# Kernel tuning notes

Measured on AMD Instinct MI355X. Metric: run time of the kernel, lower is better.

Reference implementation:

```python
import jax, jax.numpy as jnp
import numpy as np

N = 50000      # nodes
E = 400000     # edges (before self loops)
F_IN = 128     # num_features
HID = 64       # hidden_dim
HEADS = 4
G = 64         # number of graphs in batch
NCLS = 2
NEG = 0.2      # leaky relu negative slope
BN_EPS = 1e-5


def setup_inputs() -> dict:
    key = jax.random.key(0)
    ks = jax.random.split(key, 32)
    rn = lambda k, shape, s=0.05: jax.random.normal(k, shape, jnp.float32) * s
    inp = {}
    inp["x"] = jax.random.normal(ks[0], (N, F_IN), jnp.float32)
    inp["edge_index"] = jax.random.randint(ks[1], (2, E), 0, N, dtype=jnp.int32)
    inp["batch"] = jnp.sort(jax.random.randint(ks[2], (N,), 0, G, dtype=jnp.int32))
    # layer 0 GATConv (concat=True) + pre projection
    inp["conv0_W"] = rn(ks[3], (F_IN, HEADS * HID))
    inp["conv0_att_src"] = rn(ks[4], (HEADS, HID))
    inp["conv0_att_dst"] = rn(ks[5], (HEADS, HID))
    inp["conv0_bias"] = jnp.zeros((HEADS * HID,), jnp.float32)
    inp["pre0_W"] = rn(ks[6], (HEADS * HID, HID))
    inp["pre0_b"] = jnp.zeros((HID,), jnp.float32)
    # layers 1..2 GATConv (concat=False), stacked
    inp["convs_W"] = rn(ks[7], (2, HID, HEADS * HID))
    inp["convs_att_src"] = rn(ks[8], (2, HEADS, HID))
    inp["convs_att_dst"] = rn(ks[9], (2, HEADS, HID))
    inp["convs_bias"] = jnp.zeros((2, HID), jnp.float32)
    # batch norms (eval mode: running stats)
    inp["bn_gamma"] = jnp.ones((3, HID), jnp.float32)
    inp["bn_beta"] = jnp.zeros((3, HID), jnp.float32)
    inp["bn_mean"] = rn(ks[10], (3, HID), 0.1)
    inp["bn_var"] = jax.random.uniform(ks[11], (3, HID), jnp.float32) + 0.5
    # JK projection, attention pooling, classifier
    inp["jump_W"] = rn(ks[12], (3 * HID, HID))
    inp["jump_b"] = jnp.zeros((HID,), jnp.float32)
    inp["att_W"] = rn(ks[13], (HID, 1))
    inp["att_b"] = jnp.zeros((1,), jnp.float32)
    inp["cls_W1"] = rn(ks[14], (HID, HID // 2))
    inp["cls_b1"] = jnp.zeros((HID // 2,), jnp.float32)
    inp["cls_W2"] = rn(ks[15], (HID // 2, NCLS))
    inp["cls_b2"] = jnp.zeros((NCLS,), jnp.float32)
    return inp


def _segment_softmax(logits, seg, num_segments):
    m = jax.ops.segment_max(logits, seg, num_segments=num_segments)
    e = jnp.exp(logits - m[seg])
    s = jax.ops.segment_sum(e, seg, num_segments=num_segments)
    return e / s[seg]


def _gat_conv(x, src, dst, W, a_src, a_dst, bias, concat):
    n = x.shape[0]
    H, C = a_src.shape
    xh = (x @ W).reshape(n, H, C)                         # [N, H, C]
    as_n = jnp.einsum('nhc,hc->nh', xh, a_src)            # [N, H]
    ad_n = jnp.einsum('nhc,hc->nh', xh, a_dst)            # [N, H]
    logits = jax.nn.leaky_relu(as_n[src] + ad_n[dst], NEG)  # [E', H]
    att = _segment_softmax(logits, dst, n)                # softmax over incoming edges
    out = jax.ops.segment_sum(xh[src] * att[:, :, None], dst, num_segments=n)
    out = out.reshape(n, H * C) if concat else out.mean(axis=1)
    return out + bias


def _bn(h, g, b, m, v):
    return (h - m) * jax.lax.rsqrt(v + BN_EPS) * g + b


def reference(x, edge_index, batch, conv0_W, conv0_att_src, conv0_att_dst,
              conv0_bias, pre0_W, pre0_b, convs_W, convs_att_src, convs_att_dst,
              convs_bias, bn_gamma, bn_beta, bn_mean, bn_var, jump_W, jump_b,
              att_W, att_b, cls_W1, cls_b1, cls_W2, cls_b2):
    n = x.shape[0]
    loops = jnp.arange(n, dtype=edge_index.dtype)
    src = jnp.concatenate([edge_index[0], loops])         # add_self_loops=True
    dst = jnp.concatenate([edge_index[1], loops])
    reps = []
    # layer 0: concat heads -> pre projection -> BN -> ELU (no residual: 128 != 64)
    h = _gat_conv(x, src, dst, conv0_W, conv0_att_src, conv0_att_dst, conv0_bias, True)
    h = h @ pre0_W + pre0_b
    h = jax.nn.elu(_bn(h, bn_gamma[0], bn_beta[0], bn_mean[0], bn_var[0]))
    reps.append(h)
    # layers 1..2: mean heads -> BN -> ELU -> residual
    for i in range(2):
        h_in = h
        h = _gat_conv(h, src, dst, convs_W[i], convs_att_src[i], convs_att_dst[i],
                      convs_bias[i], False)
        h = jax.nn.elu(_bn(h, bn_gamma[i + 1], bn_beta[i + 1], bn_mean[i + 1], bn_var[i + 1]))
        h = h + h_in
        reps.append(h)
    # jumping knowledge (cat)
    h = jnp.concatenate(reps, axis=-1) @ jump_W + jump_b  # [N, HID]
    # attentional global pooling
    a = _segment_softmax((h @ att_W + att_b)[:, 0], batch, G)  # [N]
    hg = jax.ops.segment_sum(h * a[:, None], batch, num_segments=G)  # [G, HID]
    # classifier
    return jax.nn.relu(hg @ cls_W1 + cls_b1) @ cls_W2 + cls_b2
```

## Files before the change

kernel.cpp:

```cpp
#include <hip/hip_runtime.h>
#include <hip/hip_bf16.h>
#include <math.h>

#define NEG 0.2f
#define BNEPS 1e-5f
#define NGRAPH 64
#define SCAN_CHUNK 2048
#define POOL_BLOCKS 256

typedef short bf16x8 __attribute__((ext_vector_type(8)));
typedef float f32x4  __attribute__((ext_vector_type(4)));
typedef float f32x2  __attribute__((ext_vector_type(2)));

__device__ __forceinline__ float bf2f(unsigned short u) {
    return __uint_as_float(((unsigned)u) << 16);
}
__device__ __forceinline__ short f2bf(float f) {
    return (short)__bfloat16_as_ushort(__float2bfloat16(f));
}
__device__ __forceinline__ unsigned char f2fp8(float f) {
    int pk = __builtin_amdgcn_cvt_pk_fp8_f32(f, f, 0, false);
    return (unsigned char)(pk & 0xFF);
}

__global__ __launch_bounds__(256)
void init_kernel(const int* __restrict__ batch, int N,
                 int* __restrict__ counts, int* __restrict__ gstart,
                 float* __restrict__ hg_acc, float* __restrict__ wsum_acc,
                 const float* __restrict__ convs_W,
                 const float* __restrict__ convs_as, const float* __restrict__ convs_ad,
                 float* __restrict__ uv)
{
    int idx = blockIdx.x * 256 + threadIdx.x;
    for (int i = idx; i < N; i += gridDim.x * 256) counts[i] = 0;
    if (blockIdx.x == 0) {
        int t = threadIdx.x;
        for (int i = t; i < NGRAPH * 64; i += 256) hg_acc[i] = 0.f;
        if (t < NGRAPH) wsum_acc[t] = 0.f;
        if (t <= NGRAPH) {
            int lo = 0, hi = N;
            while (lo < hi) {
                int mid = (lo + hi) >> 1;
                if (batch[mid] < t) lo = mid + 1; else hi = mid;
            }
            gstart[t] = lo;
        }
    }
    if (blockIdx.x == 1) {
        int t = threadIdx.x;
        int h = t >> 6, k = t & 63;
        for (int i = 0; i < 2; ++i) {
            const float* Wr  = convs_W + (size_t)i * 64 * 256 + k * 256 + h * 64;
            const float* av  = convs_as + i * 256 + h * 64;
            const float* dv  = convs_ad + i * 256 + h * 64;
            float su = 0.f, sv = 0.f;
            for (int c = 0; c < 64; ++c) { su += Wr[c] * av[c]; sv += Wr[c] * dv[c]; }
            uv[i * 256 + h * 64 + k]       = su;
            uv[512 + i * 256 + h * 64 + k] = sv;
        }
    }
}

__global__ __launch_bounds__(256)
void gemm_xh_mfma(const float* __restrict__ A, int lda,
                  const float* __restrict__ W, int Nc, int M, int K,
                  const float* __restrict__ att_s, const float* __restrict__ att_d,
                  float* __restrict__ as_out, float* __restrict__ ad_out,
                  unsigned char* __restrict__ C8)
{
    __shared__ short Wt[64 * 136];
    const int KP = K + 8;
    int tid  = threadIdx.x;
    int lane = tid & 63, wave = tid >> 6;
    int row0 = blockIdx.x * 64;
    int colb = blockIdx.y * 64;
    int c15 = lane & 15, q = lane >> 4;

    {
        int n = tid & 63;
        for (int k = tid >> 6; k < K; k += 4)
            Wt[n * KP + k] = f2bf(W[(size_t)k * Nc + colb + n]);
    }
    __syncthreads();

    int row = row0 + wave * 16 + c15;
    bool rok = row < M;
    const float* arow = A + (size_t)row * lda + q * 8;

    f32x4 acc[4];
    #pragma unroll
    for (int st = 0; st < 4; ++st) acc[st] = (f32x4){0.f, 0.f, 0.f, 0.f};

    for (int k0 = 0; k0 < K; k0 += 32) {
        bf16x8 av;
        if (rok) {
            float4 a0 = *(const float4*)(arow + k0);
            float4 a1 = *(const float4*)(arow + k0 + 4);
            av[0] = f2bf(a0.x); av[1] = f2bf(a0.y); av[2] = f2bf(a0.z); av[3] = f2bf(a0.w);
            av[4] = f2bf(a1.x); av[5] = f2bf(a1.y); av[6] = f2bf(a1.z); av[7] = f2bf(a1.w);
        } else {
            av = (bf16x8){0,0,0,0,0,0,0,0};
        }
        #pragma unroll
        for (int st = 0; st < 4; ++st) {
            bf16x8 bv = *(const bf16x8*)(Wt + (st * 16 + c15) * KP + k0 + q * 8);
            acc[st] = __builtin_amdgcn_mfma_f32_16x16x32_bf16(av, bv, acc[st], 0, 0, 0);
        }
    }

    #pragma unroll
    for (int r = 0; r < 4; ++r) {
        int orow = row0 + wave * 16 + q * 4 + r;
        if (orow >= M) continue;
        unsigned char* cb = C8 + (size_t)orow * 256 + colb + c15;
        #pragma unroll
        for (int st = 0; st < 4; ++st)
            cb[st * 16] = f2fp8(acc[st][r]);
    }
    float sa[4], da[4];
    #pragma unroll
    for (int st = 0; st < 4; ++st) {
        sa[st] = att_s[colb + st * 16 + c15];
        da[st] = att_d[colb + st * 16 + c15];
    }
    #pragma unroll
    for (int r = 0; r < 4; ++r) {
        float ps = acc[0][r] * sa[0] + acc[1][r] * sa[1] + acc[2][r] * sa[2] + acc[3][r] * sa[3];
        float pd = acc[0][r] * da[0] + acc[1][r] * da[1] + acc[2][r] * da[2] + acc[3][r] * da[3];
        #pragma unroll
        for (int o = 1; o < 16; o <<= 1) {
            ps += __shfl_xor(ps, o);
            pd += __shfl_xor(pd, o);
        }
        int orow = row0 + wave * 16 + q * 4 + r;
        if (c15 == 0 && orow < M) {
            as_out[orow * 4 + blockIdx.y] = ps;
            ad_out[orow * 4 + blockIdx.y] = pd;
        }
    }
}

__global__ __launch_bounds__(256)
void gemm_n64_mfma(const void* __restrict__ Araw, int lda, int a_is_bf16,
                   const float* __restrict__ W, int w_gat, int M, int K,
                   const float* __restrict__ bias, float scale,
                   float* __restrict__ C, int ldc, int mode,
                   const float* __restrict__ bn_g, const float* __restrict__ bn_b,
                   const float* __restrict__ bn_m, const float* __restrict__ bn_v,
                   const float* __restrict__ resid, int ldr,
                   unsigned char* __restrict__ h8_out,
                   const float* __restrict__ u, const float* __restrict__ v,
                   float* __restrict__ as_out, float* __restrict__ ad_out,
                   const float* __restrict__ attW, const float* __restrict__ attb,
                   float* __restrict__ wout)
{
    __shared__ short Wt[64 * 264];
    const int KP = K + 8;
    int tid  = threadIdx.x;
    int lane = tid & 63, wave = tid >> 6;
    int row0 = blockIdx.x * 64;
    int c15 = lane & 15, q = lane >> 4;

    {
        int n = tid & 63;
        for (int k = tid >> 6; k < K; k += 4) {
            int widx = w_gat ? ((k & 63) * 256 + (k >> 6) * 64 + n) : (k * 64 + n);
            Wt[n * KP + k] = f2bf(W[widx]);
        }
    }
    __syncthreads();

    int row = row0 + wave * 16 + c15;
    bool rok = row < M;

    f32x4 acc[4];
    #pragma unroll
    for (int st = 0; st < 4; ++st) acc[st] = (f32x4){0.f, 0.f, 0.f, 0.f};

    for (int k0 = 0; k0 < K; k0 += 32) {
        bf16x8 av;
        if (rok) {
            if (a_is_bf16) {
                av = *(const bf16x8*)((const unsigned short*)Araw
                                      + (size_t)row * lda + k0 + q * 8);
            } else {
                const float* ap = (const float*)Araw + (size_t)row * lda + k0 + q * 8;
                float4 a0 = *(const float4*)ap;
                float4 a1 = *(const float4*)(ap + 4);
                av[0] = f2bf(a0.x); av[1] = f2bf(a0.y); av[2] = f2bf(a0.z); av[3] = f2bf(a0.w);
                av[4] = f2bf(a1.x); av[5] = f2bf(a1.y); av[6] = f2bf(a1.z); av[7] = f2bf(a1.w);
            }
        } else {
            av = (bf16x8){0,0,0,0,0,0,0,0};
        }
        #pragma unroll
        for (int st = 0; st < 4; ++st) {
            bf16x8 bv = *(const bf16x8*)(Wt + (st * 16 + c15) * KP + k0 + q * 8);
            acc[st] = __builtin_amdgcn_mfma_f32_16x16x32_bf16(av, bv, acc[st], 0, 0, 0);
        }
    }

    #pragma unroll
    for (int st = 0; st < 4; ++st) {
        int col = st * 16 + c15;
        float bs = bias ? bias[col] : 0.f;
        float sg = 1.f, sb = 0.f;
        if (mode == 1) {
            sg = bn_g[col] / sqrtf(bn_v[col] + BNEPS);
            sb = bn_b[col] - bn_m[col] * sg;
        }
        #pragma unroll
        for (int r = 0; r < 4; ++r) {
            int orow = row0 + wave * 16 + q * 4 + r;
            if (orow >= M) continue;
            float vvv = acc[st][r] * scale + bs;
            if (mode == 1) {
                vvv = vvv * sg + sb;
                vvv = vvv > 0.f ? vvv : __expf(vvv) - 1.f;
            }
            if (resid) vvv += resid[(size_t)orow * ldr + col];
            acc[st][r] = vvv;
            C[(size_t)orow * ldc + col] = vvv;
        }
    }

    if (h8_out) {
        #pragma unroll
        for (int r = 0; r < 4; ++r) {
            int orow = row0 + wave * 16 + q * 4 + r;
            if (orow >= M) continue;
            unsigned char* hb = h8_out + (size_t)orow * 64 + c15;
            #pragma unroll
            for (int st = 0; st < 4; ++st)
                hb[st * 16] = f2fp8(acc[st][r]);
        }
    }

    if (u) {
        float uu[4][4], vv2[4][4];
        #pragma unroll
        for (int h = 0; h < 4; ++h)
            #pragma unroll
            for (int st = 0; st < 4; ++st) {
                uu[h][st]  = u[h * 64 + st * 16 + c15];
                vv2[h][st] = v[h * 64 + st * 16 + c15];
            }
        #pragma unroll
        for (int r = 0; r < 4; ++r) {
            int orow = row0 + wave * 16 + q * 4 + r;
            float pv[8];
            #pragma unroll
            for (int h = 0; h < 4; ++h) {
                pv[h]     = acc[0][r] * uu[h][0] + acc[1][r] * uu[h][1]
                          + acc[2][r] * uu[h][2] + acc[3][r] * uu[h][3];
                pv[4 + h] = acc[0][r] * vv2[h][0] + acc[1][r] * vv2[h][1]
                          + acc[2][r] * vv2[h][2] + acc[3][r] * vv2[h][3];
            }
            #pragma unroll
            for (int j = 0; j < 4; ++j) {
                float send = (c15 & 8) ? pv[j] : pv[j + 4];
                float keep = (c15 & 8) ? pv[j + 4] : pv[j];
                pv[j] = keep + __shfl_xor(send, 8);
            }
            #pragma unroll
            for (int j = 0; j < 2; ++j) {
                float send = (c15 & 4) ? pv[j] : pv[j + 2];
                float keep = (c15 & 4) ? pv[j + 2] : pv[j];
                pv[j] = keep + __shfl_xor(send, 4);
            }
            {
                float send = (c15 & 2) ? pv[0] : pv[1];
                float keep = (c15 & 2) ? pv[1] : pv[0];
                pv[0] = keep + __shfl_xor(send, 2);
            }
            pv[0] += __shfl_xor(pv[0], 1);
            if ((c15 & 1) == 0 && orow < M) {
                int jj = c15 >> 1;
                if (jj < 4) as_out[orow * 4 + jj] = pv[0];
                else        ad_out[orow * 4 + (jj - 4)] = pv[0];
            }
        }
    }

    if (wout) {
        float sa[4];
        #pragma unroll
        for (int st = 0; st < 4; ++st) sa[st] = attW[st * 16 + c15];
        float ab = attb[0];
        #pragma unroll
        for (int r = 0; r < 4; ++r) {
            float ps = acc[0][r] * sa[0] + acc[1][r] * sa[1]
                     + acc[2][r] * sa[2] + acc[3][r] * sa[3];
            #pragma unroll
            for (int o = 1; o < 16; o <<= 1) ps += __shfl_xor(ps, o);
            int orow = row0 + wave * 16 + q * 4 + r;
            if (c15 == 0 && orow < M) wout[orow] = __expf(ps + ab);
        }
    }
}

__global__ __launch_bounds__(256)
void hist_kernel(const int* __restrict__ ei, int E, int N, int* __restrict__ counts)
{
    int e = blockIdx.x * blockDim.x + threadIdx.x;
    int Etot = E + N;
    if (e >= Etot) return;
    int d = (e < E) ? ei[E + e] : e - E;
    atomicAdd(&counts[d], 1);
}

__global__ __launch_bounds__(256)
void scan_phase1(const int* __restrict__ counts, int N, int* __restrict__ blocksum)
{
    __shared__ int wsum[4];
    int tid = threadIdx.x, lane = tid & 63, wave = tid >> 6;
    int base = blockIdx.x * SCAN_CHUNK;
    int s = 0;
    #pragma unroll
    for (int j = 0; j < SCAN_CHUNK / 256; ++j) {
        int idx = base + tid + j * 256;
        if (idx < N) s += counts[idx];
    }
    #pragma unroll
    for (int o = 32; o; o >>= 1) s += __shfl_xor(s, o);
    if (lane == 0) wsum[wave] = s;
    __syncthreads();
    if (tid == 0) blocksum[blockIdx.x] = wsum[0] + wsum[1] + wsum[2] + wsum[3];
}

__global__ __launch_bounds__(256)
void scan_phase3(const int* __restrict__ counts, int N, int nb,
                 const int* __restrict__ blocksum,
                 int* __restrict__ rowptr, int* __restrict__ cursor)
{
    __shared__ int wsum[4];
    __shared__ int pref[64];
    int tid = threadIdx.x, lane = tid & 63, wave = tid >> 6;

    if (wave == 0) {
        int v = (lane < nb) ? blocksum[lane] : 0;
        int incl = v;
        #pragma unroll
        for (int o = 1; o < 64; o <<= 1) {
            int t = __shfl_up(incl, o);
            if (lane >= o) incl += t;
        }
        pref[lane] = incl;
    }
    __syncthreads();
    int boff = blockIdx.x ? pref[blockIdx.x - 1] : 0;
    if (blockIdx.x == 0 && tid == 0) rowptr[N] = pref[nb - 1];

    int start = blockIdx.x * SCAN_CHUNK + tid * 8;
    int v[8];
    int s = 0;
    #pragma unroll
    for (int j = 0; j < 8; ++j) {
        v[j] = (start + j < N) ? counts[start + j] : 0;
        s += v[j];
    }
    int incl = s;
    #pragma unroll
    for (int o = 1; o < 64; o <<= 1) {
        int t = __shfl_up(incl, o);
        if (lane >= o) incl += t;
    }
    if (lane == 63) wsum[wave] = incl;
    __syncthreads();
    int woff = 0;
    #pragma unroll
    for (int w = 0; w < 4; ++w) if (w < wave) woff += wsum[w];
    int run = boff + woff + incl - s;
    #pragma unroll
    for (int j = 0; j < 8; ++j) {
        int idx = start + j;
        if (idx < N) { rowptr[idx] = run; cursor[idx] = run; }
        run += v[j];
    }
}

__global__ __launch_bounds__(256)
void scatter_kernel(const int* __restrict__ ei, int E, int N,
                    int* __restrict__ cursor, int* __restrict__ csr_src)
{
    int e = blockIdx.x * blockDim.x + threadIdx.x;
    int Etot = E + N;
    if (e >= Etot) return;
    int s, d;
    if (e < E) { s = ei[e]; d = ei[E + e]; } else { s = d = e - E; }
    int pos = atomicAdd(&cursor[d], 1);
    csr_src[pos] = s;
}

__global__ __launch_bounds__(256)
void aggregate_kernel(const int* __restrict__ rowptr, const int* __restrict__ csr_src,
                      const float* __restrict__ as_n, const float* __restrict__ ad_n,
                      const unsigned char* __restrict__ xh8,
                      const float* __restrict__ bias,
                      unsigned short* __restrict__ outp, int N)
{
    int node = (blockIdx.x * blockDim.x + threadIdx.x) >> 6;
    int lane = threadIdx.x & 63;
    if (node >= N) return;
    int h = lane >> 4, li = lane & 15, grp = lane & 48;
    int e0 = rowptr[node], e1 = rowptr[node + 1];
    float adh = ad_n[node * 4 + h];
    unsigned laneoff = (unsigned)(lane * 4);

    float4 acc = make_float4(0.f, 0.f, 0.f, 0.f);
    float wsum = 0.f;

    for (int base = e0; base < e1; base += 16) {
        int cnt = e1 - base; if (cnt > 16) cnt = 16;
        int s = 0; float w = 0.f;
        if (li < cnt) {
            s = csr_src[base + li];
            float l = as_n[s * 4 + h] + adh;
            l = fmaxf(l, NEG * l);
            w = __expf(l);
        }
        int k = 0;
        for (; k + 3 < cnt; k += 4) {
            float w0 = __shfl(w, grp + k),     w1 = __shfl(w, grp + k + 1);
            float w2 = __shfl(w, grp + k + 2), w3 = __shfl(w, grp + k + 3);
            int s0 = __shfl(s, grp + k),       s1 = __shfl(s, grp + k + 1);
            int s2 = __shfl(s, grp + k + 2),   s3 = __shfl(s, grp + k + 3);
            unsigned x0 = *(const unsigned*)(xh8 + ((unsigned)s0 * 256u + laneoff));
            unsigned x1 = *(const unsigned*)(xh8 + ((unsigned)s1 * 256u + laneoff));
            unsigned x2 = *(const unsigned*)(xh8 + ((unsigned)s2 * 256u + laneoff));
            unsigned x3 = *(const unsigned*)(xh8 + ((unsigned)s3 * 256u + laneoff));
            f32x2 l0 = __builtin_amdgcn_cvt_pk_f32_fp8((int)x0, false);
            f32x2 h0 = __builtin_amdgcn_cvt_pk_f32_fp8((int)x0, true);
            f32x2 l1 = __builtin_amdgcn_cvt_pk_f32_fp8((int)x1, false);
            f32x2 h1 = __builtin_amdgcn_cvt_pk_f32_fp8((int)x1, true);
            f32x2 l2 = __builtin_amdgcn_cvt_pk_f32_fp8((int)x2, false);
            f32x2 h2 = __builtin_amdgcn_cvt_pk_f32_fp8((int)x2, true);
            f32x2 l3 = __builtin_amdgcn_cvt_pk_f32_fp8((int)x3, false);
            f32x2 h3 = __builtin_amdgcn_cvt_pk_f32_fp8((int)x3, true);
            acc.x += w0 * l0.x; acc.y += w0 * l0.y; acc.z += w0 * h0.x; acc.w += w0 * h0.y;
            acc.x += w1 * l1.x; acc.y += w1 * l1.y; acc.z += w1 * h1.x; acc.w += w1 * h1.y;
            acc.x += w2 * l2.x; acc.y += w2 * l2.y; acc.z += w2 * h2.x; acc.w += w2 * h2.y;
            acc.x += w3 * l3.x; acc.y += w3 * l3.y; acc.z += w3 * h3.x; acc.w += w3 * h3.y;
            wsum += (w0 + w1) + (w2 + w3);
        }
        for (; k < cnt; ++k) {
            float wk = __shfl(w, grp + k);
            int sk = __shfl(s, grp + k);
            unsigned xv = *(const unsigned*)(xh8 + ((unsigned)sk * 256u + laneoff));
            f32x2 lo = __builtin_amdgcn_cvt_pk_f32_fp8((int)xv, false);
            f32x2 hi = __builtin_amdgcn_cvt_pk_f32_fp8((int)xv, true);
            acc.x += wk * lo.x; acc.y += wk * lo.y;
            acc.z += wk * hi.x; acc.w += wk * hi.y;
            wsum += wk;
        }
    }

    float rw = 1.f / wsum;
    float4 bs = *(const float4*)(bias + lane * 4);
    ushort4 pk;
    pk.x = (unsigned short)f2bf(acc.x * rw + bs.x);
    pk.y = (unsigned short)f2bf(acc.y * rw + bs.y);
    pk.z = (unsigned short)f2bf(acc.z * rw + bs.z);
    pk.w = (unsigned short)f2bf(acc.w * rw + bs.w);
    *(ushort4*)(outp + (size_t)node * 256 + lane * 4) = pk;
}

__global__ __launch_bounds__(256)
void aggregate_z(const int* __restrict__ rowptr, const int* __restrict__ csr_src,
                 const float* __restrict__ as_n, const float* __restrict__ ad_n,
                 const unsigned char* __restrict__ h8,
                 unsigned short* __restrict__ zout, int N)
{
    int node = (blockIdx.x * blockDim.x + threadIdx.x) >> 6;
    int lane = threadIdx.x & 63;
    if (node >= N) return;
    int h = lane >> 4, li = lane & 15, grp = lane & 48;
    int e0 = rowptr[node], e1 = rowptr[node + 1];
    float adh = ad_n[node * 4 + h];
    unsigned laneoff = (unsigned)(li * 4);

    float4 acc = make_float4(0.f, 0.f, 0.f, 0.f);
    float wsum = 0.f;

    for (int base = e0; base < e1; base += 16) {
        int cnt = e1 - base; if (cnt > 16) cnt = 16;
        int s = 0; float w = 0.f;
        if (li < cnt) {
            s = csr_src[base + li];
            float l = as_n[s * 4 + h] + adh;
            l = fmaxf(l, NEG * l);
            w = __expf(l);
        }
        int k = 0;
        for (; k + 3 < cnt; k += 4) {
            float w0 = __shfl(w, grp + k),     w1 = __shfl(w, grp + k + 1);
            float w2 = __shfl(w, grp + k + 2), w3 = __shfl(w, grp + k + 3);
            int s0 = __shfl(s, grp + k),       s1 = __shfl(s, grp + k + 1);
            int s2 = __shfl(s, grp + k + 2),   s3 = __shfl(s, grp + k + 3);
            unsigned x0 = *(const unsigned*)(h8 + ((unsigned)s0 * 64u + laneoff));
            unsigned x1 = *(const unsigned*)(h8 + ((unsigned)s1 * 64u + laneoff));
            unsigned x2 = *(const unsigned*)(h8 + ((unsigned)s2 * 64u + laneoff));
            unsigned x3 = *(const unsigned*)(h8 + ((unsigned)s3 * 64u + laneoff));
            f32x2 l0 = __builtin_amdgcn_cvt_pk_f32_fp8((int)x0, false);
            f32x2 h0 = __builtin_amdgcn_cvt_pk_f32_fp8((int)x0, true);
            f32x2 l1 = __builtin_amdgcn_cvt_pk_f32_fp8((int)x1, false);
            f32x2 h1 = __builtin_amdgcn_cvt_pk_f32_fp8((int)x1, true);
            f32x2 l2 = __builtin_amdgcn_cvt_pk_f32_fp8((int)x2, false);
            f32x2 h2 = __builtin_amdgcn_cvt_pk_f32_fp8((int)x2, true);
            f32x2 l3 = __builtin_amdgcn_cvt_pk_f32_fp8((int)x3, false);
            f32x2 h3 = __builtin_amdgcn_cvt_pk_f32_fp8((int)x3, true);
            acc.x += w0 * l0.x; acc.y += w0 * l0.y; acc.z += w0 * h0.x; acc.w += w0 * h0.y;
            acc.x += w1 * l1.x; acc.y += w1 * l1.y; acc.z += w1 * h1.x; acc.w += w1 * h1.y;
            acc.x += w2 * l2.x; acc.y += w2 * l2.y; acc.z += w2 * h2.x; acc.w += w2 * h2.y;
            acc.x += w3 * l3.x; acc.y += w3 * l3.y; acc.z += w3 * h3.x; acc.w += w3 * h3.y;
            wsum += (w0 + w1) + (w2 + w3);
        }
        for (; k < cnt; ++k) {
            float wk = __shfl(w, grp + k);
            int sk = __shfl(s, grp + k);
            unsigned xv = *(const unsigned*)(h8 + ((unsigned)sk * 64u + laneoff));
            f32x2 lo = __builtin_amdgcn_cvt_pk_f32_fp8((int)xv, false);
            f32x2 hi = __builtin_amdgcn_cvt_pk_f32_fp8((int)xv, true);
            acc.x += wk * lo.x; acc.y += wk * lo.y;
            acc.z += wk * hi.x; acc.w += wk * hi.y;
            wsum += wk;
        }
    }

    float rw = 1.f / wsum;
    ushort4 pk;
    pk.x = (unsigned short)f2bf(acc.x * rw);
    pk.y = (unsigned short)f2bf(acc.y * rw);
    pk.z = (unsigned short)f2bf(acc.z * rw);
    pk.w = (unsigned short)f2bf(acc.w * rw);
    *(ushort4*)(zout + (size_t)node * 256 + h * 64 + li * 4) = pk;
}

__global__ __launch_bounds__(256)
void pool_partial(const float* __restrict__ hjk, const float* __restrict__ w,
                  const int* __restrict__ batch, const int* __restrict__ gstart,
                  float* __restrict__ hg_acc, float* __restrict__ wsum_acc, int N)
{
    __shared__ float red[256];
    __shared__ float wred[4];
    int tid = threadIdx.x;
    int c = tid & 63, q = tid >> 6;
    int slab = (N + POOL_BLOCKS - 1) / POOL_BLOCKS;
    int n0 = blockIdx.x * slab;
    int n1 = n0 + slab; if (n1 > N) n1 = N;
    if (n0 >= n1) return;
    int g0 = batch[n0], g1 = batch[n1 - 1];

    for (int g = g0; g <= g1; ++g) {
        int s = gstart[g];     if (s < n0) s = n0;
        int e = gstart[g + 1]; if (e > n1) e = n1;
        float acc = 0.f, ws = 0.f;
        for (int n = s + q; n < e; n += 4) {
            float wn = w[n];
            acc += wn * hjk[(size_t)n * 64 + c];
            if (c == 0) ws += wn;
        }
        red[tid] = acc;
        if (c == 0) wred[q] = ws;
        __syncthreads();
        if (q == 0) {
            float v = red[c] + red[64 + c] + red[128 + c] + red[192 + c];
            if (v != 0.f) atomicAdd(&hg_acc[g * 64 + c], v);
            if (c == 0) {
                float t = wred[0] + wred[1] + wred[2] + wred[3];
                if (t != 0.f) atomicAdd(&wsum_acc[g], t);
            }
        }
        __syncthreads();
    }
}

__global__ void cls_kernel(const float* __restrict__ hg_acc,
                           const float* __restrict__ wsum_acc,
                           const float* __restrict__ W1, const float* __restrict__ b1,
                           const float* __restrict__ W2, const float* __restrict__ b2,
                           float* __restrict__ out)
{
    int g = blockIdx.x, t = threadIdx.x;
    __shared__ float z[32];
    __shared__ float h[64];
    float wsum = wsum_acc[g];
    float rw = (wsum > 0.f) ? 1.f / wsum : 0.f;
    h[t] = hg_acc[g * 64 + t] * rw;
    h[t + 32] = hg_acc[g * 64 + t + 32] * rw;
    __syncthreads();
    float acc = b1[t];
    for (int k = 0; k < 64; ++k) acc += h[k] * W1[k * 32 + t];
    z[t] = fmaxf(acc, 0.f);
    __syncthreads();
    if (t < 2) {
        float o = b2[t];
        for (int j = 0; j < 32; ++j) o += z[j] * W2[j * 2 + t];
        out[g * 2 + t] = o;
    }
}

extern "C" void kernel_launch(void* const* d_in, const int* in_sizes, int n_in,
                              void* d_out, int out_size, void* d_ws, size_t ws_size,
                              hipStream_t stream)
{
    const float* x        = (const float*)d_in[0];
    const int*   ei       = (const int*)d_in[1];
    const int*   batch    = (const int*)d_in[2];
    const float* conv0_W  = (const float*)d_in[3];
    const float* conv0_as = (const float*)d_in[4];
    const float* conv0_ad = (const float*)d_in[5];
    const float* conv0_b  = (const float*)d_in[6];
    const float* pre0_W   = (const float*)d_in[7];
    const float* pre0_b   = (const float*)d_in[8];
    const float* convs_W  = (const float*)d_in[9];
    const float* convs_as = (const float*)d_in[10];
    const float* convs_ad = (const float*)d_in[11];
    const float* convs_b  = (const float*)d_in[12];
    const float* bn_g     = (const float*)d_in[13];
    const float* bn_b     = (const float*)d_in[14];
    const float* bn_m     = (const float*)d_in[15];
    const float* bn_v     = (const float*)d_in[16];
    const float* jump_W   = (const float*)d_in[17];
    const float* jump_b   = (const float*)d_in[18];
    const float* att_W    = (const float*)d_in[19];
    const float* att_b    = (const float*)d_in[20];
    const float* cls_W1   = (const float*)d_in[21];
    const float* cls_b1   = (const float*)d_in[22];
    const float* cls_W2   = (const float*)d_in[23];
    const float* cls_b2   = (const float*)d_in[24];
    float* out = (float*)d_out;

    const int N = in_sizes[0] / 128;
    const int E = in_sizes[1] / 2;
    const int Etot = E + N;
    const int nb = (N + SCAN_CHUNK - 1) / SCAN_CHUNK;

    float* ws      = (float*)d_ws;
    unsigned char* xh8      = (unsigned char*)ws;
    unsigned short* h256_bf = (unsigned short*)ws + (size_t)N * 256;
    float* repsAll = (float*)(h256_bf + (size_t)N * 256);
    float* as_n    = repsAll + (size_t)N * 192;
    float* ad_n    = as_n + (size_t)N * 4;
    float* hjk     = ad_n + (size_t)N * 4;
    float* hg_acc  = hjk + (size_t)N * 64;
    float* wsum_acc= hg_acc + NGRAPH * 64;
    int*   rowptr  = (int*)(wsum_acc + NGRAPH);
    int*   cursor  = rowptr + (N + 1);
    int*   counts  = cursor + N;
    int*   csr_src = counts + N;
    int*   gstart  = csr_src + Etot;
    int*   blocksum = gstart + (NGRAPH + 1);
    float* uv      = (float*)(blocksum + 64);
    unsigned char* h8 = xh8;
    float* wbuf    = as_n;

    dim3 blk(256);
    int node_wave_blocks = (N + 3) / 4;
    int edge_blocks      = (Etot + 255) / 256;
    int row_blocks       = (N + 63) / 64;

    init_kernel<<<64, blk, 0, stream>>>(batch, N, counts, gstart, hg_acc, wsum_acc,
                                        convs_W, convs_as, convs_ad, uv);
    hist_kernel<<<edge_blocks, blk, 0, stream>>>(ei, E, N, counts);
    scan_phase1<<<nb, blk, 0, stream>>>(counts, N, blocksum);
    scan_phase3<<<nb, blk, 0, stream>>>(counts, N, nb, blocksum, rowptr, cursor);
    scatter_kernel<<<edge_blocks, blk, 0, stream>>>(ei, E, N, cursor, csr_src);

    {
        dim3 g1(row_blocks, 4);
        gemm_xh_mfma<<<g1, blk, 0, stream>>>(x, 128, conv0_W, 256, N, 128,
                                             conv0_as, conv0_ad, as_n, ad_n, xh8);
        aggregate_kernel<<<node_wave_blocks, blk, 0, stream>>>(
            rowptr, csr_src, as_n, ad_n, xh8, conv0_b, h256_bf, N);
        gemm_n64_mfma<<<row_blocks, blk, 0, stream>>>(
            h256_bf, 256, 1, pre0_W, 0, N, 256, pre0_b, 1.f,
            repsAll, 192, 1, bn_g, bn_b, bn_m, bn_v,
            nullptr, 0, h8, uv, uv + 512, as_n, ad_n,
            nullptr, nullptr, nullptr);
    }

    aggregate_z<<<node_wave_blocks, blk, 0, stream>>>(rowptr, csr_src, as_n, ad_n,
                                                      h8, h256_bf, N);
    gemm_n64_mfma<<<row_blocks, blk, 0, stream>>>(
        h256_bf, 256, 1, convs_W, 1, N, 256, convs_b, 0.25f,
        repsAll + 64, 192, 1, bn_g + 64, bn_b + 64, bn_m + 64, bn_v + 64,
        repsAll, 192, h8, uv + 256, uv + 512 + 256, as_n, ad_n,
        nullptr, nullptr, nullptr);

    aggregate_z<<<node_wave_blocks, blk, 0, stream>>>(rowptr, csr_src, as_n, ad_n,
                                                      h8, h256_bf, N);
    gemm_n64_mfma<<<row_blocks, blk, 0, stream>>>(
        h256_bf, 256, 1, convs_W + (size_t)64 * 256, 1, N, 256, convs_b + 64, 0.25f,
        repsAll + 128, 192, 1, bn_g + 128, bn_b + 128, bn_m + 128, bn_v + 128,
        repsAll + 64, 192, nullptr, nullptr, nullptr, nullptr, nullptr,
        nullptr, nullptr, nullptr);

    gemm_n64_mfma<<<row_blocks, blk, 0, stream>>>(
        repsAll, 192, 0, jump_W, 0, N, 192, jump_b, 1.f,
        hjk, 64, 0, nullptr, nullptr, nullptr, nullptr,
        nullptr, 0, nullptr, nullptr, nullptr, nullptr, nullptr,
        att_W, att_b, wbuf);

    pool_partial<<<POOL_BLOCKS, blk, 0, stream>>>(hjk, wbuf, batch, gstart,
                                                  hg_acc, wsum_acc, N);
    cls_kernel<<<NGRAPH, 32, 0, stream>>>(hg_acc, wsum_acc, cls_W1, cls_b1,
                                          cls_W2, cls_b2, out);
}
```

Measured before the change: 366.2 us.

## Fuse z-space aggregation with mean-head GEMM epilogue for layers one and two

Replaces the separate aggregate_z and gemm_n64 launches for the two mean-head GAT layers with one kernel. Each block aggregates 64 nodes into a shared-memory bf16 tile, then runs the MFMA GEMM with the BN/ELU/residual and attention-projection epilogue. This removes the N×256 bf16 intermediate round trip through global memory and two launches. The cost is serial per-wave aggregation of 16 nodes with less parallelism per block, large LDS use that lowers occupancy, and ping-pong h8/as/ad buffers to avoid read-write races between blocks.

New measurement: 452.7 us. 1.24x slower.

```diff
diff --git a/kernel.cpp b/kernel.cpp
--- a/kernel.cpp
+++ b/kernel.cpp
@@ -295,6 +295,195 @@
             for (int o = 1; o < 16; o <<= 1) ps += __shfl_xor(ps, o);
             int orow = row0 + wave * 16 + q * 4 + r;
             if (c15 == 0 && orow < M) wout[orow] = __expf(ps + ab);
+        }
+    }
+}
+
+__global__ __launch_bounds__(256)
+void agg_gemm_z(const int* __restrict__ rowptr, const int* __restrict__ csr_src,
+                const float* __restrict__ as_n, const float* __restrict__ ad_n,
+                const unsigned char* __restrict__ hsrc,
+                const float* __restrict__ W,
+                int M,
+                const float* __restrict__ bias, float scale,
+                float* __restrict__ C, int ldc,
+                const float* __restrict__ bn_g, const float* __restrict__ bn_b,
+                const float* __restrict__ bn_m, const float* __restrict__ bn_v,
+                const float* __restrict__ resid, int ldr,
+                unsigned char* __restrict__ h8_out,
+                const float* __restrict__ u, const float* __restrict__ v,
+                float* __restrict__ as_out, float* __restrict__ ad_out)
+{
+    __shared__ short zbuf[64 * 264];
+    __shared__ short Wt[64 * 136];
+    int tid  = threadIdx.x;
+    int lane = tid & 63, wave = tid >> 6;
+    int row0 = blockIdx.x * 64;
+    int h = lane >> 4, li = lane & 15, grp = lane & 48;
+    int c15 = lane & 15, q = lane >> 4;
+    unsigned laneoff = (unsigned)(li * 4);
+
+    for (int i = 0; i < 16; ++i) {
+        int node = row0 + wave * 16 + i;
+        int nl = wave * 16 + i;
+        float4 acc = make_float4(0.f, 0.f, 0.f, 0.f);
+        float wsum = 0.f;
+        if (node < M) {
+            float adh = ad_n[node * 4 + h];
+            int e0 = rowptr[node], e1 = rowptr[node + 1];
+            for (int base = e0; base < e1; base += 16) {
+                int cnt = e1 - base; if (cnt > 16) cnt = 16;
+                int s = 0; float w = 0.f;
+                if (li < cnt) {
+                    s = csr_src[base + li];
+                    float l = as_n[s * 4 + h] + adh;
+                    l = fmaxf(l, NEG * l);
+                    w = __expf(l);
+                }
+                int k = 0;
+                for (; k + 3 < cnt; k += 4) {
+                    float w0 = __shfl(w, grp + k),     w1 = __shfl(w, grp + k + 1);
+                    float w2 = __shfl(w, grp + k + 2), w3 = __shfl(w, grp + k + 3);
+                    int s0 = __shfl(s, grp + k),       s1 = __shfl(s, grp + k + 1);
+                    int s2 = __shfl(s, grp + k + 2),   s3 = __shfl(s, grp + k + 3);
+                    unsigned x0 = *(const unsigned*)(hsrc + ((unsigned)s0 * 64u + laneoff));
+                    unsigned x1 = *(const unsigned*)(hsrc + ((unsigned)s1 * 64u + laneoff));
+                    unsigned x2 = *(const unsigned*)(hsrc + ((unsigned)s2 * 64u + laneoff));
+                    unsigned x3 = *(const unsigned*)(hsrc + ((unsigned)s3 * 64u + laneoff));
+                    f32x2 l0 = __builtin_amdgcn_cvt_pk_f32_fp8((int)x0, false);
+                    f32x2 h0 = __builtin_amdgcn_cvt_pk_f32_fp8((int)x0, true);
+                    f32x2 l1 = __builtin_amdgcn_cvt_pk_f32_fp8((int)x1, false);
+                    f32x2 h1 = __builtin_amdgcn_cvt_pk_f32_fp8((int)x1, true);
+                    f32x2 l2 = __builtin_amdgcn_cvt_pk_f32_fp8((int)x2, false);
+                    f32x2 h2 = __builtin_amdgcn_cvt_pk_f32_fp8((int)x2, true);
+                    f32x2 l3 = __builtin_amdgcn_cvt_pk_f32_fp8((int)x3, false);
+                    f32x2 h3 = __builtin_amdgcn_cvt_pk_f32_fp8((int)x3, true);
+                    acc.x += w0 * l0.x; acc.y += w0 * l0.y; acc.z += w0 * h0.x; acc.w += w0 * h0.y;
+                    acc.x += w1 * l1.x; acc.y += w1 * l1.y; acc.z += w1 * h1.x; acc.w += w1 * h1.y;
+                    acc.x += w2 * l2.x; acc.y += w2 * l2.y; acc.z += w2 * h2.x; acc.w += w2 * h2.y;
+                    acc.x += w3 * l3.x; acc.y += w3 * l3.y; acc.z += w3 * h3.x; acc.w += w3 * h3.y;
+                    wsum += (w0 + w1) + (w2 + w3);
+                }
+                for (; k < cnt; ++k) {
+                    float wk = __shfl(w, grp + k);
+                    int sk = __shfl(s, grp + k);
+                    unsigned xv = *(const unsigned*)(hsrc + ((unsigned)sk * 64u + laneoff));
+                    f32x2 lo = __builtin_amdgcn_cvt_pk_f32_fp8((int)xv, false);
+                    f32x2 hi = __builtin_amdgcn_cvt_pk_f32_fp8((int)xv, true);
+                    acc.x += wk * lo.x; acc.y += wk * lo.y;
+                    acc.z += wk * hi.x; acc.w += wk * hi.y;
+                    wsum += wk;
+                }
+            }
+        }
+        float rw = (wsum > 0.f) ? 1.f / wsum : 0.f;
+        ushort4 pk;
+        pk.x = (unsigned short)f2bf(acc.x * rw);
+        pk.y = (unsigned short)f2bf(acc.y * rw);
+        pk.z = (unsigned short)f2bf(acc.z * rw);
+        pk.w = (unsigned short)f2bf(acc.w * rw);
+        *(ushort4*)((unsigned short*)zbuf + nl * 264 + lane * 4) = pk;
+    }
+
+    f32x4 acc2[4];
+    #pragma unroll
+    for (int st = 0; st < 4; ++st) acc2[st] = (f32x4){0.f, 0.f, 0.f, 0.f};
+
+    for (int kh = 0; kh < 2; ++kh) {
+        __syncthreads();
+        {
+            int n = tid & 63;
+            for (int k = tid >> 6; k < 128; k += 4) {
+                int kk = kh * 128 + k;
+                Wt[n * 136 + k] = f2bf(W[(kk & 63) * 256 + (kk >> 6) * 64 + n]);
+            }
+        }
+        __syncthreads();
+        const unsigned short* zb = (const unsigned short*)zbuf;
+        for (int k0 = 0; k0 < 128; k0 += 32) {
+            bf16x8 av = *(const bf16x8*)(zb + (wave * 16 + c15) * 264 + kh * 128 + k0 + q * 8);
+            #pragma unroll
+            for (int st = 0; st < 4; ++st) {
+                bf16x8 bv = *(const bf16x8*)(Wt + (st * 16 + c15) * 136 + k0 + q * 8);
+                acc2[st] = __builtin_amdgcn_mfma_f32_16x16x32_bf16(av, bv, acc2[st], 0, 0, 0);
+            }
+        }
+    }
+
+    #pragma unroll
+    for (int st = 0; st < 4; ++st) {
+        int col = st * 16 + c15;
+        float bs = bias[col];
+        float sg = bn_g[col] / sqrtf(bn_v[col] + BNEPS);
+        float sb = bn_b[col] - bn_m[col] * sg;
+        #pragma unroll
+        for (int r = 0; r < 4; ++r) {
+            int orow = row0 + wave * 16 + q * 4 + r;
+            if (orow >= M) continue;
+            float vvv = acc2[st][r] * scale + bs;
+            vvv = vvv * sg + sb;
+            vvv = vvv > 0.f ? vvv : __expf(vvv) - 1.f;
+            vvv += resid[(size_t)orow * ldr + col];
+            acc2[st][r] = vvv;
+            C[(size_t)orow * ldc + col] = vvv;
+        }
+    }
+
+    if (h8_out) {
+        #pragma unroll
+        for (int r = 0; r < 4; ++r) {
+            int orow = row0 + wave * 16 + q * 4 + r;
+            if (orow >= M) continue;
+            unsigned char* hb = h8_out + (size_t)orow * 64 + c15;
+            #pragma unroll
+            for (int st = 0; st < 4; ++st)
+                hb[st * 16] = f2fp8(acc2[st][r]);
+        }
+    }
+
+    if (u) {
+        float uu[4][4], vv2[4][4];
+        #pragma unroll
+        for (int hh = 0; hh < 4; ++hh)
+            #pragma unroll
+            for (int st = 0; st < 4; ++st) {
+                uu[hh][st]  = u[hh * 64 + st * 16 + c15];
+                vv2[hh][st] = v[hh * 64 + st * 16 + c15];
+            }
+        #pragma unroll
+        for (int r = 0; r < 4; ++r) {
+            int orow = row0 + wave * 16 + q * 4 + r;
+            float pv[8];
+            #pragma unroll
+            for (int hh = 0; hh < 4; ++hh) {
+                pv[hh]     = acc2[0][r] * uu[hh][0] + acc2[1][r] * uu[hh][1]
+                           + acc2[2][r] * uu[hh][2] + acc2[3][r] * uu[hh][3];
+                pv[4 + hh] = acc2[0][r] * vv2[hh][0] + acc2[1][r] * vv2[hh][1]
+                           + acc2[2][r] * vv2[hh][2] + acc2[3][r] * vv2[hh][3];
+            }
+            #pragma unroll
+            for (int j = 0; j < 4; ++j) {
+                float send = (c15 & 8) ? pv[j] : pv[j + 4];
+                float keep = (c15 & 8) ? pv[j + 4] : pv[j];
+                pv[j] = keep + __shfl_xor(send, 8);
+            }
+            #pragma unroll
+            for (int j = 0; j < 2; ++j) {
+                float send = (c15 & 4) ? pv[j] : pv[j + 2];
+                float keep = (c15 & 4) ? pv[j + 2] : pv[j];
+                pv[j] = keep + __shfl_xor(send, 4);
+            }
+            {
+                float send = (c15 & 2) ? pv[0] : pv[1];
+                float keep = (c15 & 2) ? pv[1] : pv[0];
+                pv[0] = keep + __shfl_xor(send, 2);
+            }
+            pv[0] += __shfl_xor(pv[0], 1);
+            if ((c15 & 1) == 0 && orow < M) {
+                int jj = c15 >> 1;
+                if (jj < 4) as_out[orow * 4 + jj] = pv[0];
+                else        ad_out[orow * 4 + (jj - 4)] = pv[0];
+            }
         }
     }
 }
@@ -463,77 +652,6 @@
     pk.z = (unsigned short)f2bf(acc.z * rw + bs.z);
     pk.w = (unsigned short)f2bf(acc.w * rw + bs.w);
     *(ushort4*)(outp + (size_t)node * 256 + lane * 4) = pk;
-}
-
-__global__ __launch_bounds__(256)
-void aggregate_z(const int* __restrict__ rowptr, const int* __restrict__ csr_src,
-                 const float* __restrict__ as_n, const float* __restrict__ ad_n,
-                 const unsigned char* __restrict__ h8,
-                 unsigned short* __restrict__ zout, int N)
-{
-    int node = (blockIdx.x * blockDim.x + threadIdx.x) >> 6;
-    int lane = threadIdx.x & 63;
-    if (node >= N) return;
-    int h = lane >> 4, li = lane & 15, grp = lane & 48;
-    int e0 = rowptr[node], e1 = rowptr[node + 1];
-    float adh = ad_n[node * 4 + h];
-    unsigned laneoff = (unsigned)(li * 4);
-
-    float4 acc = make_float4(0.f, 0.f, 0.f, 0.f);
-    float wsum = 0.f;
-
-    for (int base = e0; base < e1; base += 16) {
-        int cnt = e1 - base; if (cnt > 16) cnt = 16;
-        int s = 0; float w = 0.f;
-        if (li < cnt) {
-            s = csr_src[base + li];
-            float l = as_n[s * 4 + h] + adh;
-            l = fmaxf(l, NEG * l);
-            w = __expf(l);
-        }
-        int k = 0;
-        for (; k + 3 < cnt; k += 4) {
-            float w0 = __shfl(w, grp + k),     w1 = __shfl(w, grp + k + 1);
-            float w2 = __shfl(w, grp + k + 2), w3 = __shfl(w, grp + k + 3);
-            int s0 = __shfl(s, grp + k),       s1 = __shfl(s, grp + k + 1);
-            int s2 = __shfl(s, grp + k + 2),   s3 = __shfl(s, grp + k + 3);
-            unsigned x0 = *(const unsigned*)(h8 + ((unsigned)s0 * 64u + laneoff));
-            unsigned x1 = *(const unsigned*)(h8 + ((unsigned)s1 * 64u + laneoff));
-            unsigned x2 = *(const unsigned*)(h8 + ((unsigned)s2 * 64u + laneoff));
-            unsigned x3 = *(const unsigned*)(h8 + ((unsigned)s3 * 64u + laneoff));
-            f32x2 l0 = __builtin_amdgcn_cvt_pk_f32_fp8((int)x0, false);
-            f32x2 h0 = __builtin_amdgcn_cvt_pk_f32_fp8((int)x0, true);
-            f32x2 l1 = __builtin_amdgcn_cvt_pk_f32_fp8((int)x1, false);
-            f32x2 h1 = __builtin_amdgcn_cvt_pk_f32_fp8((int)x1, true);
-            f32x2 l2 = __builtin_amdgcn_cvt_pk_f32_fp8((int)x2, false);
-            f32x2 h2 = __builtin_amdgcn_cvt_pk_f32_fp8((int)x2, true);
-            f32x2 l3 = __builtin_amdgcn_cvt_pk_f32_fp8((int)x3, false);
-            f32x2 h3 = __builtin_amdgcn_cvt_pk_f32_fp8((int)x3, true);
-            acc.x += w0 * l0.x; acc.y += w0 * l0.y; acc.z += w0 * h0.x; acc.w += w0 * h0.y;
-            acc.x += w1 * l1.x; acc.y += w1 * l1.y; acc.z += w1 * h1.x; acc.w += w1 * h1.y;
-            acc.x += w2 * l2.x; acc.y += w2 * l2.y; acc.z += w2 * h2.x; acc.w += w2 * h2.y;
-            acc.x += w3 * l3.x; acc.y += w3 * l3.y; acc.z += w3 * h3.x; acc.w += w3 * h3.y;
-            wsum += (w0 + w1) + (w2 + w3);
-        }
-        for (; k < cnt; ++k) {
-            float wk = __shfl(w, grp + k);
-            int sk = __shfl(s, grp + k);
-            unsigned xv = *(const unsigned*)(h8 + ((unsigned)sk * 64u + laneoff));
-            f32x2 lo = __builtin_amdgcn_cvt_pk_f32_fp8((int)xv, false);
-            f32x2 hi = __builtin_amdgcn_cvt_pk_f32_fp8((int)xv, true);
-            acc.x += wk * lo.x; acc.y += wk * lo.y;
-            acc.z += wk * hi.x; acc.w += wk * hi.y;
-            wsum += wk;
-        }
-    }
-
-    float rw = 1.f / wsum;
-    ushort4 pk;
-    pk.x = (unsigned short)f2bf(acc.x * rw);
-    pk.y = (unsigned short)f2bf(acc.y * rw);
-    pk.z = (unsigned short)f2bf(acc.z * rw);
-    pk.w = (unsigned short)f2bf(acc.w * rw);
-    *(ushort4*)(zout + (size_t)node * 256 + h * 64 + li * 4) = pk;
 }
 
 __global__ __launch_bounds__(256)
@@ -652,7 +770,10 @@
     int*   gstart  = csr_src + Etot;
     int*   blocksum = gstart + (NGRAPH + 1);
     float* uv      = (float*)(blocksum + 64);
-    unsigned char* h8 = xh8;
+    float* as2     = uv + 1024;
+    float* ad2     = as2 + (size_t)N * 4;
+    unsigned char* h8b = (unsigned char*)(ad2 + (size_t)N * 4);
+    unsigned char* h8a = xh8;
     float* wbuf    = as_n;
 
     dim3 blk(256);
@@ -676,25 +797,25 @@
         gemm_n64_mfma<<<row_blocks, blk, 0, stream>>>(
             h256_bf, 256, 1, pre0_W, 0, N, 256, pre0_b, 1.f,
             repsAll, 192, 1, bn_g, bn_b, bn_m, bn_v,
-            nullptr, 0, h8, uv, uv + 512, as_n, ad_n,
+            nullptr, 0, h8a, uv, uv + 512, as_n, ad_n,
             nullptr, nullptr, nullptr);
     }
 
-    aggregate_z<<<node_wave_blocks, blk, 0, stream>>>(rowptr, csr_src, as_n, ad_n,
-                                                      h8, h256_bf, N);
-    gemm_n64_mfma<<<row_blocks, blk, 0, stream>>>(
-        h256_bf, 256, 1, convs_W, 1, N, 256, convs_b, 0.25f,
-        repsAll + 64, 192, 1, bn_g + 64, bn_b + 64, bn_m + 64, bn_v + 64,
-        repsAll, 192, h8, uv + 256, uv + 512 + 256, as_n, ad_n,
-        nullptr, nullptr, nullptr);
-
-    aggregate_z<<<node_wave_blocks, blk, 0, stream>>>(rowptr, csr_src, as_n, ad_n,
-                                                      h8, h256_bf, N);
-    gemm_n64_mfma<<<row_blocks, blk, 0, stream>>>(
-        h256_bf, 256, 1, convs_W + (size_t)64 * 256, 1, N, 256, convs_b + 64, 0.25f,
-        repsAll + 128, 192, 1, bn_g + 128, bn_b + 128, bn_m + 128, bn_v + 128,
-        repsAll + 64, 192, nullptr, nullptr, nullptr, nullptr, nullptr,
-        nullptr, nullptr, nullptr);
+    agg_gemm_z<<<row_blocks, blk, 0, stream>>>(
+        rowptr, csr_src, as_n, ad_n, h8a,
+        convs_W, N, convs_b, 0.25f,
+        repsAll + 64, 192,
+        bn_g + 64, bn_b + 64, bn_m + 64, bn_v + 64,
+        repsAll, 192,
+        h8b, uv + 256, uv + 512 + 256, as2, ad2);
+
+    agg_gemm_z<<<row_blocks, blk, 0, stream>>>(
+        rowptr, csr_src, as2, ad2, h8b,
+        convs_W + (size_t)64 * 256, N, convs_b + 64, 0.25f,
+        repsAll + 128, 192,
+        bn_g + 128, bn_b + 128, bn_m + 128, bn_v + 128,
+        repsAll + 64, 192,
+        nullptr, nullptr, nullptr, nullptr, nullptr);
 
     gemm_n64_mfma<<<row_blocks, blk, 0, stream>>>(
         repsAll, 192, 0, jump_W, 0, N, 192, jump_b, 1.f,
```

## Fuse attentional pooling into JK GEMM epilogue and drop pool kernel

Applied to the files above, without the earlier changes.

The pooling step now happens inside the final jump-knowledge GEMM epilogue. That epilogue computes the exp attention weight, then atomically adds weighted rows into per-graph accumulators. When all rows in a wave share a graph, it first reduces across the wave with shuffles. This removes the hjk intermediate write and read, and one kernel launch. It also double-buffers the fp8 features and attention logits between layers, apparently to avoid aliasing once hjk is gone. The cost is more global float atomics on 64x64 accumulators, which adds contention.

Measured after the change: 433.4 us. 18.4% more time.

```diff
diff --git a/kernel.cpp b/kernel.cpp
--- a/kernel.cpp
+++ b/kernel.cpp
@@ -6,7 +6,6 @@
 #define BNEPS 1e-5f
 #define NGRAPH 64
 #define SCAN_CHUNK 2048
-#define POOL_BLOCKS 256
 
 typedef short bf16x8 __attribute__((ext_vector_type(8)));
 typedef float f32x4  __attribute__((ext_vector_type(4)));
@@ -152,7 +151,8 @@
                    const float* __restrict__ u, const float* __restrict__ v,
                    float* __restrict__ as_out, float* __restrict__ ad_out,
                    const float* __restrict__ attW, const float* __restrict__ attb,
-                   float* __restrict__ wout)
+                   const int* __restrict__ batch,
+                   float* __restrict__ hg_acc, float* __restrict__ wsum_acc)
 {
     __shared__ short Wt[64 * 264];
     const int KP = K + 8;
@@ -220,7 +220,7 @@
             }
             if (resid) vvv += resid[(size_t)orow * ldr + col];
             acc[st][r] = vvv;
-            C[(size_t)orow * ldc + col] = vvv;
+            if (C) C[(size_t)orow * ldc + col] = vvv;
         }
     }
 
@@ -282,19 +282,45 @@
         }
     }
 
-    if (wout) {
+    if (attW) {
         float sa[4];
         #pragma unroll
         for (int st = 0; st < 4; ++st) sa[st] = attW[st * 16 + c15];
         float ab = attb[0];
         #pragma unroll
         for (int r = 0; r < 4; ++r) {
+            int orow = row0 + wave * 16 + q * 4 + r;
+            bool ok = orow < M;
             float ps = acc[0][r] * sa[0] + acc[1][r] * sa[1]
                      + acc[2][r] * sa[2] + acc[3][r] * sa[3];
             #pragma unroll
             for (int o = 1; o < 16; o <<= 1) ps += __shfl_xor(ps, o);
-            int orow = row0 + wave * 16 + q * 4 + r;
-            if (c15 == 0 && orow < M) wout[orow] = __expf(ps + ab);
+            float w = __expf(ps + ab);
+            int g = ok ? batch[orow] : -1;
+            int mn = g, mx = g;
+            { int t1 = __shfl_xor(mn, 16); mn = min(mn, t1); t1 = __shfl_xor(mx, 16); mx = max(mx, t1); }
+            { int t1 = __shfl_xor(mn, 32); mn = min(mn, t1); t1 = __shfl_xor(mx, 32); mx = max(mx, t1); }
+            bool uni = (mn == mx) && (mn >= 0);
+            #pragma unroll
+            for (int st = 0; st < 4; ++st) {
+                float vv = ok ? acc[st][r] * w : 0.f;
+                float vq = vv + __shfl_xor(vv, 16);
+                vq += __shfl_xor(vq, 32);
+                int col = st * 16 + c15;
+                if (uni) {
+                    if (q == 0) atomicAdd(&hg_acc[g * 64 + col], vq);
+                } else if (ok) {
+                    atomicAdd(&hg_acc[g * 64 + col], vv);
+                }
+            }
+            float wv = (ok && c15 == 0) ? w : 0.f;
+            float wq = wv + __shfl_xor(wv, 16);
+            wq += __shfl_xor(wq, 32);
+            if (uni) {
+                if (q == 0 && c15 == 0) atomicAdd(&wsum_acc[g], wq);
+            } else if (ok && c15 == 0) {
+                atomicAdd(&wsum_acc[g], wv);
+            }
         }
     }
 }
@@ -534,45 +560,6 @@
     pk.z = (unsigned short)f2bf(acc.z * rw);
     pk.w = (unsigned short)f2bf(acc.w * rw);
     *(ushort4*)(zout + (size_t)node * 256 + h * 64 + li * 4) = pk;
-}
-
-__global__ __launch_bounds__(256)
-void pool_partial(const float* __restrict__ hjk, const float* __restrict__ w,
-                  const int* __restrict__ batch, const int* __restrict__ gstart,
-                  float* __restrict__ hg_acc, float* __restrict__ wsum_acc, int N)
-{
-    __shared__ float red[256];
-    __shared__ float wred[4];
-    int tid = threadIdx.x;
-    int c = tid & 63, q = tid >> 6;
-    int slab = (N + POOL_BLOCKS - 1) / POOL_BLOCKS;
-    int n0 = blockIdx.x * slab;
-    int n1 = n0 + slab; if (n1 > N) n1 = N;
-    if (n0 >= n1) return;
-    int g0 = batch[n0], g1 = batch[n1 - 1];
-
-    for (int g = g0; g <= g1; ++g) {
-        int s = gstart[g];     if (s < n0) s = n0;
-        int e = gstart[g + 1]; if (e > n1) e = n1;
-        float acc = 0.f, ws = 0.f;
-        for (int n = s + q; n < e; n += 4) {
-            float wn = w[n];
-            acc += wn * hjk[(size_t)n * 64 + c];
-            if (c == 0) ws += wn;
-        }
-        red[tid] = acc;
-        if (c == 0) wred[q] = ws;
-        __syncthreads();
-        if (q == 0) {
-            float v = red[c] + red[64 + c] + red[128 + c] + red[192 + c];
-            if (v != 0.f) atomicAdd(&hg_acc[g * 64 + c], v);
-            if (c == 0) {
-                float t = wred[0] + wred[1] + wred[2] + wred[3];
-                if (t != 0.f) atomicAdd(&wsum_acc[g], t);
-            }
-        }
-        __syncthreads();
-    }
 }
 
 __global__ void cls_kernel(const float* __restrict__ hg_acc,
@@ -642,8 +629,7 @@
     float* repsAll = (float*)(h256_bf + (size_t)N * 256);
     float* as_n    = repsAll + (size_t)N * 192;
     float* ad_n    = as_n + (size_t)N * 4;
-    float* hjk     = ad_n + (size_t)N * 4;
-    float* hg_acc  = hjk + (size_t)N * 64;
+    float* hg_acc  = ad_n + (size_t)N * 4;
     float* wsum_acc= hg_acc + NGRAPH * 64;
     int*   rowptr  = (int*)(wsum_acc + NGRAPH);
     int*   cursor  = rowptr + (N + 1);
@@ -652,8 +638,10 @@
     int*   gstart  = csr_src + Etot;
     int*   blocksum = gstart + (NGRAPH + 1);
     float* uv      = (float*)(blocksum + 64);
-    unsigned char* h8 = xh8;
-    float* wbuf    = as_n;
+    float* as2     = uv + 1024;
+    float* ad2     = as2 + (size_t)N * 4;
+    unsigned char* h8b = (unsigned char*)(ad2 + (size_t)N * 4);
+    unsigned char* h8a = xh8;
 
     dim3 blk(256);
     int node_wave_blocks = (N + 3) / 4;
@@ -676,34 +664,32 @@
         gemm_n64_mfma<<<row_blocks, blk, 0, stream>>>(
             h256_bf, 256, 1, pre0_W, 0, N, 256, pre0_b, 1.f,
             repsAll, 192, 1, bn_g, bn_b, bn_m, bn_v,
-            nullptr, 0, h8, uv, uv + 512, as_n, ad_n,
-            nullptr, nullptr, nullptr);
+            nullptr, 0, h8a, uv, uv + 512, as_n, ad_n,
+            nullptr, nullptr, nullptr, nullptr, nullptr);
     }
 
     aggregate_z<<<node_wave_blocks, blk, 0, stream>>>(rowptr, csr_src, as_n, ad_n,
-                                                      h8, h256_bf, N);
+                                                      h8a, h256_bf, N);
     gemm_n64_mfma<<<row_blocks, blk, 0, stream>>>(
         h256_bf, 256, 1, convs_W, 1, N, 256, convs_b, 0.25f,
         repsAll + 64, 192, 1, bn_g + 64, bn_b + 64, bn_m + 64, bn_v + 64,
-        repsAll, 192, h8, uv + 256, uv + 512 + 256, as_n, ad_n,
-        nullptr, nullptr, nullptr);
-
-    aggregate_z<<<node_wave_blocks, blk, 0, stream>>>(rowptr, csr_src, as_n, ad_n,
-                                                      h8, h256_bf, N);
+        repsAll, 192, h8b, uv + 256, uv + 512 + 256, as2, ad2,
+        nullptr, nullptr, nullptr, nullptr, nullptr);
+
+    aggregate_z<<<node_wave_blocks, blk, 0, stream>>>(rowptr, csr_src, as2, ad2,
+                                                      h8b, h256_bf, N);
     gemm_n64_mfma<<<row_blocks, blk, 0, stream>>>(
         h256_bf, 256, 1, convs_W + (size_t)64 * 256, 1, N, 256, convs_b + 64, 0.25f,
         repsAll + 128, 192, 1, bn_g + 128, bn_b + 128, bn_m + 128, bn_v + 128,
         repsAll + 64, 192, nullptr, nullptr, nullptr, nullptr, nullptr,
-        nullptr, nullptr, nullptr);
+        nullptr, nullptr, nullptr, nullptr, nullptr);
 
     gemm_n64_mfma<<<row_blocks, blk, 0, stream>>>(
         repsAll, 192, 0, jump_W, 0, N, 192, jump_b, 1.f,
-        hjk, 64, 0, nullptr, nullptr, nullptr, nullptr,
+        nullptr, 64, 0, nullptr, nullptr, nullptr, nullptr,
         nullptr, 0, nullptr, nullptr, nullptr, nullptr, nullptr,
-        att_W, att_b, wbuf);
-
-    pool_partial<<<POOL_BLOCKS, blk, 0, stream>>>(hjk, wbuf, batch, gstart,
-                                                  hg_acc, wsum_acc, N);
+        att_W, att_b, batch, hg_acc, wsum_acc);
+
     cls_kernel<<<NGRAPH, 32, 0, stream>>>(hg_acc, wsum_acc, cls_W1, cls_b1,
                                           cls_W2, cls_b2, out);
 }
```
